# Kernel optimization log

Measured on AMD Instinct MI355X. Metric: run time of the kernel, lower is better.

Reference implementation:

```python
import jax, jax.numpy as jnp
import numpy as np

B = 16; Hp = 24; Wp = 24; N = Hp * Wp + 2  # 578 = patches + cls + freq tokens
D = 768; H = 12; HDIM = D // H
BAND = 64; SD = 16  # sd = min(16, max(4, band_dim))
HID = 3072  # int(embed_dim * mlp_ratio)
SCALE = HDIM ** -0.5; CLIP = 10.0
FILM_SCALE = 0.5; SPEC_INIT = 0.02; GATE_INIT = 0.05


def _ln(x, w, b, eps=1e-6):
    m = jnp.mean(x, axis=-1, keepdims=True)
    v = jnp.mean((x - m) ** 2, axis=-1, keepdims=True)
    return (x - m) * jax.lax.rsqrt(v + eps) * w + b


def _rms(x, eps=1e-6):
    return x * jax.lax.rsqrt(jnp.mean(x * x, axis=-1, keepdims=True) + eps)


def setup_inputs() -> dict:
    key = jax.random.key(0)
    ks = jax.random.split(key, 16)
    rn = lambda k, s, sc=1.0: jax.random.normal(k, s, dtype=jnp.float32) * sc
    return {
        "x": rn(ks[0], (B, N, D)),
        "band_tokens": rn(ks[1], (B, 1, D)),  # unused by forward (matches torch signature)
        "freq_token_for_cond": rn(ks[2], (B, 1, D)),
        "freq_summary": rn(ks[3], (B, D)),
        "token_band_feat": rn(ks[4], (B, N, BAND)),
        "alpha": jnp.ones((1,), jnp.float32),
        "ln_gate_w": jnp.ones((D,), jnp.float32), "ln_gate_b": jnp.zeros((D,), jnp.float32),
        "film_w": rn(ks[5], (D, 2 * D), 1e-4), "film_b": jnp.zeros((2 * D,), jnp.float32),
        "ln_attn_w": jnp.ones((D,), jnp.float32), "ln_attn_b": jnp.zeros((D,), jnp.float32),
        "qkv_w": rn(ks[6], (D, 3 * D), 0.02), "qkv_b": jnp.zeros((3 * D,), jnp.float32),
        "proj_w": rn(ks[7], (D, D), 0.02), "proj_b": jnp.zeros((D,), jnp.float32),
        "spec_bias_scale": jnp.float32(SPEC_INIT),
        "gate_w": rn(ks[8], (D, H), 1e-4), "gate_b": jnp.zeros((H,), jnp.float32),
        "band_proj_w": rn(ks[9], (BAND, SD), 0.02),
        "ln_mlp_w": jnp.ones((D,), jnp.float32), "ln_mlp_b": jnp.zeros((D,), jnp.float32),
        "fc1_w": rn(ks[10], (D, HID), 0.02), "fc1_b": jnp.zeros((HID,), jnp.float32),
        "fc2_w": rn(ks[11], (HID, D), 0.02), "fc2_b": jnp.zeros((D,), jnp.float32),
        "dw_w": rn(ks[12], (HID, 1, 3, 3), 0.1), "dw_b": jnp.zeros((HID,), jnp.float32),
    }


def _forward(x, band_tokens, freq_token_for_cond, freq_summary, token_band_feat, alpha,
             ln_gate_w, ln_gate_b, film_w, film_b, ln_attn_w, ln_attn_b,
             qkv_w, qkv_b, proj_w, proj_b, spec_bias_scale, gate_w, gate_b, band_proj_w,
             ln_mlp_w, ln_mlp_b, fc1_w, fc1_b, fc2_w, fc2_b, dw_w, dw_b):
    a = alpha.reshape(())
    # --- FiLM gate on patch tokens (replaces patch, no residual) ---
    cls_freq = x[:, :2]
    patch = x[:, 2:]
    p = _ln(patch, ln_gate_w, ln_gate_b)
    gb = freq_summary @ film_w + film_b            # [B, 2D]
    gamma, beta = jnp.split(gb, 2, axis=-1)
    gamma = jnp.tanh(gamma) * FILM_SCALE
    beta = jnp.tanh(beta) * FILM_SCALE
    patch = p * (1.0 + a * gamma[:, None, :]) + a * beta[:, None, :]
    x = jnp.concatenate([cls_freq, patch], axis=1)
    # --- spectral-similarity attention ---
    xn = _ln(x, ln_attn_w, ln_attn_b)
    qkv = (xn @ qkv_w + qkv_b).reshape(B, N, 3, H, HDIM)
    q = _rms(qkv[:, :, 0].transpose(0, 2, 1, 3))   # [B,H,N,hd]
    k = _rms(qkv[:, :, 1].transpose(0, 2, 1, 3))
    v = qkv[:, :, 2].transpose(0, 2, 1, 3)
    logits = jnp.einsum('bhnd,bhmd->bhnm', q * SCALE, k)
    s = _rms(token_band_feat @ band_proj_w)        # [B,N,SD]
    ssim = jnp.einsum('bns,bms->bnm', s, s)        # [B,N,N]
    logits = jnp.clip(logits + a * spec_bias_scale * ssim[:, None], -CLIP, CLIP)
    attn = jax.nn.softmax(logits, axis=-1)
    out = jnp.einsum('bhnm,bhmd->bhnd', attn, v)
    g = jnp.tanh(freq_token_for_cond[:, 0] @ gate_w + gate_b) * GATE_INIT  # [B,H]
    out = out * (1.0 + a * g[:, :, None, None])
    out = out.transpose(0, 2, 1, 3).reshape(B, N, D)
    x = x + (out @ proj_w + proj_b)
    # --- conv MLP on patch tokens only ---
    cls_freq = x[:, :2]
    patch = x[:, 2:]
    h = jax.nn.gelu(_ln(patch, ln_mlp_w, ln_mlp_b) @ fc1_w + fc1_b, approximate=False)
    h = h.transpose(0, 2, 1).reshape(B, HID, Hp, Wp)
    h = jax.lax.conv_general_dilated(h, dw_w, (1, 1), 'SAME', feature_group_count=HID,
                                     dimension_numbers=('NCHW', 'OIHW', 'NCHW'))
    h = jax.nn.silu(h + dw_b[None, :, None, None])
    h = h.reshape(B, HID, Hp * Wp).transpose(0, 2, 1)
    patch = patch + (h @ fc2_w + fc2_b)
    return jnp.concatenate([cls_freq, patch], axis=1)


def reference(x, band_tokens, freq_token_for_cond, freq_summary, token_band_feat, alpha,
              ln_gate_w, ln_gate_b, film_w, film_b, ln_attn_w, ln_attn_b,
              qkv_w, qkv_b, proj_w, proj_b, spec_bias_scale, gate_w, gate_b, band_proj_w,
              ln_mlp_w, ln_mlp_b, fc1_w, fc1_b, fc2_w, fc2_b, dw_w, dw_b):
    return _forward(x, band_tokens, freq_token_for_cond, freq_summary, token_band_feat, alpha,
                    ln_gate_w, ln_gate_b, film_w, film_b, ln_attn_w, ln_attn_b,
                    qkv_w, qkv_b, proj_w, proj_b, spec_bias_scale, gate_w, gate_b, band_proj_w,
                    ln_mlp_w, ln_mlp_b, fc1_w, fc1_b, fc2_w, fc2_b, dw_w, dw_b)
```

## Files before the change

kernel.cpp:

```cpp
#include <hip/hip_runtime.h>
#include <hip/hip_bf16.h>

#define BATCH 16
#define NTOK 578
#define NTOKP 592
#define NP 576
#define PGRID 24
#define DIM 768
#define NH 12
#define HDIM 64
#define BAND 64
#define SDIM 16
#define HID 3072
#define SCALE 0.125f
#define CLIPV 10.0f
#define KHS 104
#define VTS 72
#define PLS 72
#define FKS 16

typedef __attribute__((ext_vector_type(8))) short bf16x8;
typedef __attribute__((ext_vector_type(4))) float f32x4;

__device__ __forceinline__ float b2f(short u) {
  union { float f; unsigned int i; } x;
  x.i = ((unsigned int)(unsigned short)u) << 16;
  return x.f;
}
__device__ __forceinline__ short f2b(float x) {
  __hip_bfloat16 h = __float2bfloat16(x);
  return *reinterpret_cast<short*>(&h);
}

__device__ __forceinline__ void gload16(const short* g, short* l) {
  __builtin_amdgcn_global_load_lds(
      (const __attribute__((address_space(1))) unsigned int*)g,
      (__attribute__((address_space(3))) unsigned int*)l, 16, 0, 0);
}

__device__ __forceinline__ int swz_wgid(int orig, int nwg) {
  int xcd = orig & 7, i = orig >> 3;
  int q = nwg >> 3, r = nwg & 7;
  return (xcd < r) ? xcd * (q + 1) + i : r * (q + 1) + (xcd - r) * q + i;
}

__device__ __forceinline__ void block_reduce2(float& a, float& b) {
  __shared__ float sm[8];
  #pragma unroll
  for (int o = 32; o > 0; o >>= 1) { a += __shfl_down(a, o); b += __shfl_down(b, o); }
  int lane = threadIdx.x & 63, w = threadIdx.x >> 6;
  __syncthreads();
  if (lane == 0) { sm[w] = a; sm[4 + w] = b; }
  __syncthreads();
  a = sm[0] + sm[1] + sm[2] + sm[3];
  b = sm[4] + sm[5] + sm[6] + sm[7];
}

#define TKS 266
__device__ __forceinline__ void tw2(
    const float* __restrict__ W, short* __restrict__ Wt, int K, int N,
    int kblk, int nblk, short* t) {
  int tid = threadIdx.x;
  int k0 = kblk * 256, n0 = nblk * 64;
  int r0 = tid >> 4, c0 = (tid & 15) * 4;
  #pragma unroll
  for (int it = 0; it < 16; it++) {
    int r = it * 16 + r0;
    float4 v = *(const float4*)(W + (size_t)(k0 + r) * N + n0 + c0);
    t[(c0 + 0) * TKS + r] = f2b(v.x);
    t[(c0 + 1) * TKS + r] = f2b(v.y);
    t[(c0 + 2) * TKS + r] = f2b(v.z);
    t[(c0 + 3) * TKS + r] = f2b(v.w);
  }
  __syncthreads();
  int n1 = tid >> 5, k1 = (tid & 31) * 8;
  #pragma unroll
  for (int it = 0; it < 8; it++) {
    int n = it * 8 + n1;
    *(bf16x8*)(Wt + (size_t)(n0 + n) * K + k0 + k1) = *(bf16x8*)(t + n * TKS + k1);
  }
}

__global__ __launch_bounds__(256) void prep_weights(
    const float* __restrict__ qkv_w, const float* __restrict__ proj_w,
    const float* __restrict__ fc1_w, const float* __restrict__ fc2_w,
    const float* __restrict__ dww,
    short* __restrict__ qkvT, short* __restrict__ projT,
    short* __restrict__ fc1T, short* __restrict__ fc2T, float* __restrict__ dwt) {
  __shared__ short t[64 * TKS];
  int id = blockIdx.x;
  if (id < 108) {
    tw2(qkv_w, qkvT, 768, 2304, id % 3, id / 3, t);
  } else if (id < 144) {
    int u = id - 108; tw2(proj_w, projT, 768, 768, u % 3, u / 3, t);
  } else if (id < 288) {
    int u = id - 144; tw2(fc1_w, fc1T, 768, 3072, u % 3, u / 3, t);
  } else if (id < 432) {
    int u = id - 288; tw2(fc2_w, fc2T, 3072, 768, u % 12, u / 12, t);
  } else {
    int i = (id - 432) * 256 + threadIdx.x;
    if (i < 9 * HID) { int tt = i / HID, c = i - tt * HID; dwt[i] = dww[c * 9 + tt]; }
  }
}

__global__ __launch_bounds__(256) void film_part(
    const float* __restrict__ fsum, const float* __restrict__ film_w,
    float* __restrict__ part) {
  __shared__ float fs[BATCH][48];
  int bid = blockIdx.x;
  int cg = bid % 12, ks = bid / 12;
  int tid = threadIdx.x;
  int k0 = ks * 48;
  for (int i = tid; i < BATCH * 48; i += 256) {
    int b = i / 48, kk = i - b * 48;
    fs[b][kk] = fsum[b * DIM + k0 + kk];
  }
  __syncthreads();
  int col4 = cg * 128 + (tid & 31) * 4;
  int bq = tid >> 5;
  float a0[4] = {0.f, 0.f, 0.f, 0.f}, a1[4] = {0.f, 0.f, 0.f, 0.f};
  #pragma unroll 4
  for (int kk = 0; kk < 48; kk++) {
    float4 w = *(const float4*)(film_w + (size_t)(k0 + kk) * 2 * DIM + col4);
    float f0 = fs[bq][kk], f1 = fs[bq + 8][kk];
    a0[0] += f0 * w.x; a0[1] += f0 * w.y; a0[2] += f0 * w.z; a0[3] += f0 * w.w;
    a1[0] += f1 * w.x; a1[1] += f1 * w.y; a1[2] += f1 * w.z; a1[3] += f1 * w.w;
  }
  *(float4*)(part + ((size_t)ks * BATCH + bq) * 1536 + col4) =
      (float4){a0[0], a0[1], a0[2], a0[3]};
  *(float4*)(part + ((size_t)ks * BATCH + bq + 8) * 1536 + col4) =
      (float4){a1[0], a1[1], a1[2], a1[3]};
}

__global__ __launch_bounds__(256) void film_fin(
    const float* __restrict__ part, const float* __restrict__ film_b,
    const float* __restrict__ ftc, const float* __restrict__ gate_w,
    const float* __restrict__ gate_b,
    float* __restrict__ gamma, float* __restrict__ beta, float* __restrict__ g) {
  int bid = blockIdx.x;
  if (bid < 96) {
    int idx = bid * 256 + threadIdx.x;
    int b = idx / 1536, col = idx - b * 1536;
    float acc = film_b[col];
    #pragma unroll
    for (int ks = 0; ks < FKS; ks++)
      acc += part[((size_t)ks * BATCH + b) * 1536 + col];
    float t = tanhf(acc) * 0.5f;
    if (col < DIM) gamma[b * DIM + col] = t;
    else beta[b * DIM + (col - DIM)] = t;
  } else {
    int widx = (bid - 96) * 4 + (threadIdx.x >> 6);
    int lane = threadIdx.x & 63;
    if (widx < BATCH * NH) {
      int b = widx / NH, h = widx - b * NH;
      float acc = 0.f;
      for (int kk = lane; kk < DIM; kk += 64) acc += ftc[b * DIM + kk] * gate_w[kk * NH + h];
      #pragma unroll
      for (int o = 32; o > 0; o >>= 1) acc += __shfl_down(acc, o);
      if (lane == 0) g[widx] = tanhf(acc + gate_b[h]) * 0.05f;
    }
  }
}

__global__ __launch_bounds__(256) void band_s_kernel(
    const float* __restrict__ tbf, const float* __restrict__ bw, float* __restrict__ s) {
  int row = blockIdx.x * 4 + (threadIdx.x >> 6);
  int lane = threadIdx.x & 63;
  if (row >= BATCH * NTOK) return;
  const float* t = tbf + (size_t)row * BAND;
  float val = 0.f;
  if (lane < SDIM) {
    for (int i = 0; i < BAND; i++) val += t[i] * bw[i * SDIM + lane];
  }
  float ss = val * val;
  #pragma unroll
  for (int o = 8; o > 0; o >>= 1) ss += __shfl_xor(ss, o, 16);
  if (lane < SDIM) s[(size_t)row * SDIM + lane] = val * rsqrtf(ss * (1.f / 16.f) + 1e-6f);
}

__global__ __launch_bounds__(256) void transpose_v(
    const short* __restrict__ v, short* __restrict__ vT) {
  __shared__ short t[64][72];
  int bh = blockIdx.y;
  int n0 = blockIdx.x * 64;
  int tid = threadIdx.x;
  const short* vb = v + (size_t)bh * NTOK * HDIM;
  short* ob = vT + (size_t)bh * HDIM * NTOKP;
  {
    int r = tid >> 2, c0 = (tid & 3) * 16;
    int n = n0 + r;
    bf16x8 a0 = {0,0,0,0,0,0,0,0}, a1 = {0,0,0,0,0,0,0,0};
    if (n < NTOK) {
      a0 = *(const bf16x8*)(vb + (size_t)n * HDIM + c0);
      a1 = *(const bf16x8*)(vb + (size_t)n * HDIM + c0 + 8);
    }
    *(bf16x8*)(&t[r][c0]) = a0;
    *(bf16x8*)(&t[r][c0 + 8]) = a1;
  }
  __syncthreads();
  {
    int d = tid & 63, nc = tid >> 6;
    int nbase = n0 + nc * 16;
    short tmp[16];
    #pragma unroll
    for (int e = 0; e < 16; e++) tmp[e] = t[nc * 16 + e][d];
    if (nbase + 16 <= NTOK) {
      *(bf16x8*)(ob + (size_t)d * NTOKP + nbase) = *(bf16x8*)tmp;
      *(bf16x8*)(ob + (size_t)d * NTOKP + nbase + 8) = *(bf16x8*)(tmp + 8);
    } else {
      for (int e = 0; e < 16; e++)
        if (nbase + e < NTOK) ob[(size_t)d * NTOKP + nbase + e] = tmp[e];
    }
  }
}

__global__ __launch_bounds__(256) void ln_film_kernel(
    const float* __restrict__ x, const float* __restrict__ gamma, const float* __restrict__ beta,
    const float* __restrict__ gw, const float* __restrict__ gb,
    const float* __restrict__ aw, const float* __restrict__ ab,
    const float* __restrict__ alpha, float* __restrict__ xw, __hip_bfloat16* __restrict__ xn) {
  int row = blockIdx.x;
  int b = row / NTOK, n = row % NTOK;
  int tid = threadIdx.x;
  const float* xr = x + (size_t)row * DIM;
  float vals[3];
  #pragma unroll
  for (int j = 0; j < 3; j++) vals[j] = xr[tid + j * 256];
  if (n >= 2) {
    float s = vals[0] + vals[1] + vals[2];
    float ss = vals[0]*vals[0] + vals[1]*vals[1] + vals[2]*vals[2];
    block_reduce2(s, ss);
    float mean = s * (1.f / 768.f);
    float inv = rsqrtf(ss * (1.f / 768.f) - mean * mean + 1e-6f);
    float a = alpha[0];
    #pragma unroll
    for (int j = 0; j < 3; j++) {
      int d = tid + j * 256;
      float p = (vals[j] - mean) * inv * gw[d] + gb[d];
      vals[j] = p * (1.f + a * gamma[(size_t)b * DIM + d]) + a * beta[(size_t)b * DIM + d];
    }
  }
  float* xwr = xw + (size_t)row * DIM;
  #pragma unroll
  for (int j = 0; j < 3; j++) xwr[tid + j * 256] = vals[j];
  float s = vals[0] + vals[1] + vals[2];
  float ss = vals[0]*vals[0] + vals[1]*vals[1] + vals[2]*vals[2];
  block_reduce2(s, ss);
  float mean = s * (1.f / 768.f);
  float inv = rsqrtf(ss * (1.f / 768.f) - mean * mean + 1e-6f);
  __hip_bfloat16* xnr = xn + (size_t)row * DIM;
  #pragma unroll
  for (int j = 0; j < 3; j++) {
    int d = tid + j * 256;
    xnr[d] = __float2bfloat16((vals[j] - mean) * inv * aw[d] + ab[d]);
  }
}

__device__ __forceinline__ void stage_tile256(
    const short* __restrict__ A, const short* __restrict__ Wt, int K,
    int m0, int n0, int kt, short* Al, short* Bl, int wid, int lrow, int lcolsw) {
  #pragma unroll
  for (int it = 0; it < 4; it++) {
    int r0 = wid * 8 + it * 64;
    gload16(A + (size_t)(m0 + r0 + lrow) * K + kt + lcolsw, Al + r0 * 64);
  }
  #pragma unroll
  for (int it = 0; it < 2; it++) {
    int r0 = wid * 8 + it * 64;
    gload16(Wt + (size_t)(n0 + r0 + lrow) * K + kt + lcolsw, Bl + r0 * 64);
  }
}

__device__ __forceinline__ void compute_tile256(
    const short* Al, const short* Bl, f32x4 acc[4][4],
    int wr, int wc, int ln15, int kb) {
  int rx = ln15 & 7;
  #pragma unroll
  for (int kk = 0; kk < 2; kk++) {
    int csw = ((kk * 4 + kb) ^ rx) * 8;
    bf16x8 af[4], bfr[4];
    #pragma unroll
    for (int i = 0; i < 4; i++)
      af[i] = *(const bf16x8*)(Al + (wr * 64 + i * 16 + ln15) * 64 + csw);
    #pragma unroll
    for (int j = 0; j < 4; j++)
      bfr[j] = *(const bf16x8*)(Bl + (wc * 64 + j * 16 + ln15) * 64 + csw);
    #pragma unroll
    for (int i = 0; i < 4; i++)
      #pragma unroll
      for (int j = 0; j < 4; j++)
        acc[i][j] = __builtin_amdgcn_mfma_f32_16x16x32_bf16(af[i], bfr[j], acc[i][j], 0, 0, 0);
  }
}

__device__ __forceinline__ void mfma_core_256(
    const short* __restrict__ A, const short* __restrict__ Wt,
    int K, int m0, int n0, f32x4 acc[4][4], short* Al, short* Bl) {
  int tid = threadIdx.x, lane = tid & 63, wid = tid >> 6;
  int wr = wid >> 1, wc = wid & 1;
  int ln15 = lane & 15, kb = lane >> 4;
  int lrow = lane >> 3;
  int lcolsw = (((lane & 7) ^ lrow) & 7) * 8;
  #pragma unroll
  for (int i = 0; i < 4; i++)
    #pragma unroll
    for (int j = 0; j < 4; j++) acc[i][j] = (f32x4){0.f, 0.f, 0.f, 0.f};
  for (int kt = 0; kt < K; kt += 64) {
    stage_tile256(A, Wt, K, m0, n0, kt, Al, Bl, wid, lrow, lcolsw);
    __syncthreads();
    compute_tile256(Al, Bl, acc, wr, wc, ln15, kb);
    __syncthreads();
  }
}

__device__ __forceinline__ void stage_tile64(
    const short* __restrict__ A, const short* __restrict__ Wt, int K,
    int m0, int n0, int kt, short* Al, short* Bl, int wid, int lrow, int lcolsw) {
  #pragma unroll
  for (int it = 0; it < 2; it++) {
    int r0 = wid * 8 + it * 32;
    gload16(A + (size_t)(m0 + r0 + lrow) * K + kt + lcolsw, Al + r0 * 64);
  }
  #pragma unroll
  for (int it = 0; it < 4; it++) {
    int r0 = wid * 8 + it * 32;
    gload16(Wt + (size_t)(n0 + r0 + lrow) * K + kt + lcolsw, Bl + r0 * 64);
  }
}

__device__ __forceinline__ void compute_tile64(
    const short* Al, const short* Bl, f32x4 acc[4][2],
    int wid, int ln15, int kb) {
  int rx = ln15 & 7;
  #pragma unroll
  for (int kk = 0; kk < 2; kk++) {
    int csw = ((kk * 4 + kb) ^ rx) * 8;
    bf16x8 af[4], bfr[2];
    #pragma unroll
    for (int i = 0; i < 4; i++)
      af[i] = *(const bf16x8*)(Al + (i * 16 + ln15) * 64 + csw);
    #pragma unroll
    for (int j = 0; j < 2; j++)
      bfr[j] = *(const bf16x8*)(Bl + (wid * 32 + j * 16 + ln15) * 64 + csw);
    #pragma unroll
    for (int i = 0; i < 4; i++)
      #pragma unroll
      for (int j = 0; j < 2; j++)
        acc[i][j] = __builtin_amdgcn_mfma_f32_16x16x32_bf16(af[i], bfr[j], acc[i][j], 0, 0, 0);
  }
}

__device__ __forceinline__ void mfma_core_64(
    const short* __restrict__ A, const short* __restrict__ Wt,
    int K, int m0, int n0, f32x4 acc[4][2],
    short* Al0, short* Bl0, short* Al1, short* Bl1) {
  int tid = threadIdx.x, lane = tid & 63, wid = tid >> 6;
  int ln15 = lane & 15, kb = lane >> 4;
  int lrow = lane >> 3;
  int lcolsw = (((lane & 7) ^ lrow) & 7) * 8;
  #pragma unroll
  for (int i = 0; i < 4; i++)
    #pragma unroll
    for (int j = 0; j < 2; j++) acc[i][j] = (f32x4){0.f, 0.f, 0.f, 0.f};
  stage_tile64(A, Wt, K, m0, n0, 0, Al0, Bl0, wid, lrow, lcolsw);
  stage_tile64(A, Wt, K, m0, n0, 64, Al1, Bl1, wid, lrow, lcolsw);
  asm volatile("s_waitcnt vmcnt(6)" ::: "memory");
  __builtin_amdgcn_s_barrier();
  const int NKT = K >> 6;
  for (int t = 0; t < NKT; t++) {
    const short* Ac = (t & 1) ? Al1 : Al0;
    const short* Bc = (t & 1) ? Bl1 : Bl0;
    compute_tile64(Ac, Bc, acc, wid, ln15, kb);
    __builtin_amdgcn_s_barrier();
    if (t + 2 < NKT) {
      short* As = (t & 1) ? Al1 : Al0;
      short* Bs = (t & 1) ? Bl1 : Bl0;
      stage_tile64(A, Wt, K, m0, n0, (t + 2) << 6, As, Bs, wid, lrow, lcolsw);
      asm volatile("s_waitcnt vmcnt(6)" ::: "memory");
    } else if (t + 1 < NKT) {
      asm volatile("s_waitcnt vmcnt(0)" ::: "memory");
    }
    __builtin_amdgcn_s_barrier();
  }
}

__global__ __launch_bounds__(512) void gemm_qkv(
    const short* __restrict__ A, const short* __restrict__ Wt, const float* __restrict__ bias,
    __hip_bfloat16* __restrict__ q, __hip_bfloat16* __restrict__ k, __hip_bfloat16* __restrict__ v) {
  __shared__ short Al[256 * 64], Bl[128 * 64];
  f32x4 acc[4][4];
  int wgid = swz_wgid(blockIdx.x, 37 * 18);
  int m0 = (wgid % 37) * 256, n0 = (wgid / 37) * 128;
  mfma_core_256(A, Wt, DIM, m0, n0, acc, Al, Bl);
  int tid = threadIdx.x, lane = tid & 63, wid = tid >> 6, wr = wid >> 1, wc = wid & 1;
  int ln15 = lane & 15, lq = lane >> 4;
  int colbase = n0 + wc * 64;
  int which = colbase / DIM;
  int rem = colbase - which * DIM;
  int h = rem >> 6;
  __hip_bfloat16* dst = (which == 0) ? q : ((which == 1) ? k : v);
  float fin_scale = (which == 0) ? SCALE : 1.0f;
  float bv[4];
  #pragma unroll
  for (int j = 0; j < 4; j++) bv[j] = bias[colbase + j * 16 + ln15];
  #pragma unroll
  for (int i = 0; i < 4; i++) {
    #pragma unroll
    for (int r = 0; r < 4; r++) {
      int m = m0 + wr * 64 + i * 16 + lq * 4 + r;
      float v4[4];
      #pragma unroll
      for (int j = 0; j < 4; j++) v4[j] = acc[i][j][r] + bv[j];
      float inv = fin_scale;
      if (which < 2) {
        float ss = v4[0]*v4[0] + v4[1]*v4[1] + v4[2]*v4[2] + v4[3]*v4[3];
        ss += __shfl_xor(ss, 1); ss += __shfl_xor(ss, 2);
        ss += __shfl_xor(ss, 4); ss += __shfl_xor(ss, 8);
        inv = rsqrtf(ss * (1.f / 64.f) + 1e-6f) * fin_scale;
      }
      if (m < BATCH * NTOK) {
        int b = m / NTOK, n = m - b * NTOK;
        __hip_bfloat16* orow = dst + (((size_t)b * NH + h) * NTOK + n) * HDIM;
        #pragma unroll
        for (int j = 0; j < 4; j++)
          orow[j * 16 + ln15] = __float2bfloat16(v4[j] * inv);
      }
    }
  }
}

__global__ __launch_bounds__(512) void attn_mfma(
    const short* __restrict__ q, const short* __restrict__ k,
    const short* __restrict__ vT, const float* __restrict__ s,
    const float* __restrict__ g, const float* __restrict__ alpha,
    const float* __restrict__ sbs, short* __restrict__ ao) {
  __shared__ short Kh[64 * KHS];
  __shared__ short Vt[2][64 * VTS];
  __shared__ short Pl[8][16 * PLS];
  int xcd = blockIdx.x & 7, idx = blockIdx.x >> 3;
  int bh = xcd * 24 + idx / 5;
  int n0 = (idx % 5) * 128;
  int b = bh / NH, h = bh - b * NH;
  int tid = threadIdx.x, lane = tid & 63, w = tid >> 6;
  int l15 = lane & 15, lg = lane >> 4;
  float a = alpha[0], c = a * sbs[0];
  const short* qb = q + (size_t)bh * NTOK * HDIM;
  const short* kb = k + (size_t)bh * NTOK * HDIM;
  const short* vtb = vT + (size_t)bh * HDIM * NTOKP;
  const float* sb = s + (size_t)b * NTOK * SDIM;
  const bf16x8 Z8 = {0, 0, 0, 0, 0, 0, 0, 0};

  int qrow = n0 + w * 16 + l15;
  int qsrc = (qrow < NTOK) ? qrow : 0;
  bf16x8 qf0 = *(const bf16x8*)(qb + (size_t)qsrc * HDIM + lg * 8);
  bf16x8 qf1 = *(const bf16x8*)(qb + (size_t)qsrc * HDIM + 32 + lg * 8);
  bf16x8 qf2 = Z8;
  if (lg < 2) {
    const float* sp = sb + (size_t)qsrc * SDIM + lg * 8;
    #pragma unroll
    for (int j = 0; j < 8; j++) qf2[j] = f2b(c * sp[j]);
  }

  f32x4 accO[4];
  #pragma unroll
  for (int dd = 0; dd < 4; dd++) accO[dd] = (f32x4){0.f, 0.f, 0.f, 0.f};
  float rsum[4] = {0.f, 0.f, 0.f, 0.f};

  int srow = (tid & 255) >> 2, sseg = tid & 3;
  if (tid < 256 && sseg == 3) {
    short* dst = Kh + srow * KHS + 80;
    *(bf16x8*)dst = Z8;
    *(bf16x8*)(dst + 8) = Z8;
  }

  auto stageK = [&](int mt) {
    int key = mt + srow;
    bool kok = key < NTOK;
    if (sseg < 2) {
      bf16x8 v0 = Z8, v1 = Z8, v2 = Z8, v3 = Z8;
      if (kok) {
        const short* src = kb + (size_t)key * HDIM + sseg * 32;
        v0 = *(const bf16x8*)(src);
        v1 = *(const bf16x8*)(src + 8);
        v2 = *(const bf16x8*)(src + 16);
        v3 = *(const bf16x8*)(src + 24);
      }
      short* dst = Kh + srow * KHS + sseg * 32;
      *(bf16x8*)dst = v0;
      *(bf16x8*)(dst + 8) = v1;
      *(bf16x8*)(dst + 16) = v2;
      *(bf16x8*)(dst + 24) = v3;
    } else if (sseg == 2) {
      bf16x8 v0 = Z8, v1 = Z8;
      if (kok) {
        const float* sp = sb + (size_t)key * SDIM;
        #pragma unroll
        for (int j = 0; j < 8; j++) { v0[j] = f2b(sp[j]); v1[j] = f2b(sp[j + 8]); }
      }
      short* dst = Kh + srow * KHS + 64;
      *(bf16x8*)dst = v0;
      *(bf16x8*)(dst + 8) = v1;
    }
  };
  auto stageV = [&](int mt, short* VtB) {
    int kk0 = sseg * 16;
    short* dst = VtB + srow * VTS + kk0;
    const short* src = vtb + (size_t)srow * NTOKP + mt + kk0;
    if (mt + kk0 + 16 <= NTOK) {
      *(bf16x8*)dst = *(const bf16x8*)src;
      *(bf16x8*)(dst + 8) = *(const bf16x8*)(src + 8);
    } else {
      for (int e = 0; e < 16; e++)
        dst[e] = (mt + kk0 + e < NTOK) ? src[e] : (short)0;
    }
  };

  if (tid < 256) stageK(0); else stageV(0, Vt[0]);
  __syncthreads();
  const int NT = 10;
  for (int ti = 0; ti < NT; ti++) {
    int mt = ti * 64, cur = ti & 1;
    const short* VtC = Vt[cur];
    f32x4 sa[4];
    __builtin_amdgcn_s_setprio(1);
    #pragma unroll
    for (int jj = 0; jj < 4; jj++) {
      sa[jj] = (f32x4){0.f, 0.f, 0.f, 0.f};
      const short* kp = Kh + (jj * 16 + l15) * KHS + lg * 8;
      sa[jj] = __builtin_amdgcn_mfma_f32_16x16x32_bf16(qf0, *(const bf16x8*)kp, sa[jj], 0, 0, 0);
      sa[jj] = __builtin_amdgcn_mfma_f32_16x16x32_bf16(qf1, *(const bf16x8*)(kp + 32), sa[jj], 0, 0, 0);
      sa[jj] = __builtin_amdgcn_mfma_f32_16x16x32_bf16(qf2, *(const bf16x8*)(kp + 64), sa[jj], 0, 0, 0);
    }
    __builtin_amdgcn_s_setprio(0);
    __syncthreads();
    if (ti + 1 < NT) {
      if (tid < 256) stageK(mt + 64);
      else stageV(mt + 64, Vt[cur ^ 1]);
    }
    short* pw = Pl[w];
    float ps[4][4];
    #pragma unroll
    for (int jj = 0; jj < 4; jj++) {
      bool ok = (mt + jj * 16 + l15) < NTOK;
      #pragma unroll
      for (int r = 0; r < 4; r++) {
        float x = sa[jj][r];
        x = fminf(fmaxf(x, -CLIPV), CLIPV);
        float e = ok ? __expf(x) : 0.f;
        ps[jj][r] = e;
        pw[(lg * 4 + r) * PLS + jj * 16 + l15] = f2b(e);
      }
    }
    #pragma unroll
    for (int r = 0; r < 4; r++) {
      float t = ps[0][r] + ps[1][r] + ps[2][r] + ps[3][r];
      t += __shfl_xor(t, 1); t += __shfl_xor(t, 2);
      t += __shfl_xor(t, 4); t += __shfl_xor(t, 8);
      rsum[r] += t;
    }
    __builtin_amdgcn_s_setprio(1);
    #pragma unroll
    for (int kc = 0; kc < 2; kc++) {
      bf16x8 pa = *(const bf16x8*)(pw + l15 * PLS + kc * 32 + lg * 8);
      #pragma unroll
      for (int dd = 0; dd < 4; dd++) {
        bf16x8 vf = *(const bf16x8*)(VtC + (dd * 16 + l15) * VTS + kc * 32 + lg * 8);
        accO[dd] = __builtin_amdgcn_mfma_f32_16x16x32_bf16(pa, vf, accO[dd], 0, 0, 0);
      }
    }
    __builtin_amdgcn_s_setprio(0);
    __syncthreads();
  }
  float gm = 1.f + a * g[bh];
  #pragma unroll
  for (int r = 0; r < 4; r++) {
    int n = n0 + w * 16 + lg * 4 + r;
    if (n >= NTOK) continue;
    float inv = gm / rsum[r];
    short* orow = ao + ((size_t)b * NTOK + n) * DIM + h * HDIM;
    #pragma unroll
    for (int dd = 0; dd < 4; dd++)
      orow[dd * 16 + l15] = f2b(accO[dd][r] * inv);
  }
}

__global__ __launch_bounds__(256) void gemm_proj(
    const short* __restrict__ A, const short* __restrict__ Wt, const float* __restrict__ bias,
    float* __restrict__ xw, float* __restrict__ out) {
  __shared__ short Al0[64 * 64], Bl0[128 * 64], Al1[64 * 64], Bl1[128 * 64];
  f32x4 acc[4][2];
  int wgid = swz_wgid(blockIdx.x, 145 * 6);
  int m0 = (wgid % 145) * 64, n0 = (wgid / 145) * 128;
  mfma_core_64(A, Wt, DIM, m0, n0, acc, Al0, Bl0, Al1, Bl1);
  int tid = threadIdx.x, lane = tid & 63, wid = tid >> 6;
  int ln15 = lane & 15, lq = lane >> 4;
  #pragma unroll
  for (int i = 0; i < 4; i++) {
    #pragma unroll
    for (int j = 0; j < 2; j++) {
      int col = n0 + wid * 32 + j * 16 + ln15;
      float bv = bias[col];
      #pragma unroll
      for (int r = 0; r < 4; r++) {
        int m = m0 + i * 16 + lq * 4 + r;
        if (m >= BATCH * NTOK) continue;
        int n = m % NTOK;
        float val = acc[i][j][r] + bv + xw[(size_t)m * DIM + col];
        xw[(size_t)m * DIM + col] = val;
        if (n < 2) out[(size_t)m * DIM + col] = val;
      }
    }
  }
}

__global__ __launch_bounds__(256) void ln_mlp_kernel(
    const float* __restrict__ x2, const float* __restrict__ w, const float* __restrict__ bb,
    __hip_bfloat16* __restrict__ xm) {
  int r = blockIdx.x;
  int b = r / NP, pi = r % NP;
  int tid = threadIdx.x;
  const float* xr = x2 + ((size_t)b * NTOK + 2 + pi) * DIM;
  float vals[3];
  #pragma unroll
  for (int j = 0; j < 3; j++) vals[j] = xr[tid + j * 256];
  float s = vals[0] + vals[1] + vals[2];
  float ss = vals[0]*vals[0] + vals[1]*vals[1] + vals[2]*vals[2];
  block_reduce2(s, ss);
  float mean = s * (1.f / 768.f);
  float inv = rsqrtf(ss * (1.f / 768.f) - mean * mean + 1e-6f);
  __hip_bfloat16* xo = xm + (size_t)r * DIM;
  #pragma unroll
  for (int j = 0; j < 3; j++) {
    int d = tid + j * 256;
    xo[d] = __float2bfloat16((vals[j] - mean) * inv * w[d] + bb[d]);
  }
}

__global__ __launch_bounds__(512) void gemm_fc1(
    const short* __restrict__ A, const short* __restrict__ Wt, const float* __restrict__ bias,
    __hip_bfloat16* __restrict__ h1) {
  __shared__ short Al[256 * 64], Bl[128 * 64];
  f32x4 acc[4][4];
  int wgid = swz_wgid(blockIdx.x, 18 * 24);
  int m0 = (wgid % 18) * 256, n0 = (wgid / 18) * 128;
  mfma_core_256(A, Wt, DIM, m0, n0, acc, Al, Bl);
  int tid = threadIdx.x, lane = tid & 63, wid = tid >> 6, wr = wid >> 1, wc = wid & 1;
  int ln15 = lane & 15, lq = lane >> 4;
  #pragma unroll
  for (int i = 0; i < 4; i++) {
    #pragma unroll
    for (int j = 0; j < 4; j++) {
      int col = n0 + wc * 64 + j * 16 + ln15;
      float bv = bias[col];
      #pragma unroll
      for (int r = 0; r < 4; r++) {
        int m = m0 + wr * 64 + i * 16 + lq * 4 + r;
        float val = acc[i][j][r] + bv;
        float ge = 0.5f * val * (1.f + erff(val * 0.70710678118f));
        h1[(size_t)m * HID + col] = __float2bfloat16(ge);
      }
    }
  }
}

__global__ __launch_bounds__(256) void dwconv_kernel(
    const __hip_bfloat16* __restrict__ h1, const float* __restrict__ dwt,
    const float* __restrict__ dwb, __hip_bfloat16* __restrict__ h2) {
  int gx = blockIdx.x;
  int b = gx / 144, g = gx - b * 144;
  int y = g / 6, x0 = (g - y * 6) * 4;
  int tid = threadIdx.x;
  int c0 = blockIdx.y * 512 + (tid & 63) * 8;
  int x = x0 + (tid >> 6);
  const short* in = (const short*)h1 + (size_t)b * NP * HID + c0;
  bf16x8 iv[3][3];
  #pragma unroll
  for (int ky = 0; ky < 3; ky++) {
    int yy = y + ky - 1;
    #pragma unroll
    for (int kx = 0; kx < 3; kx++) {
      int xx = x + kx - 1;
      bool ok = (yy >= 0 && yy < PGRID && xx >= 0 && xx < PGRID);
      iv[ky][kx] = ok ? *(const bf16x8*)(in + (size_t)(yy * PGRID + xx) * HID)
                      : (bf16x8){0, 0, 0, 0, 0, 0, 0, 0};
    }
  }
  float acc[8];
  {
    float4 b0 = *(const float4*)(dwb + c0);
    float4 b1 = *(const float4*)(dwb + c0 + 4);
    acc[0] = b0.x; acc[1] = b0.y; acc[2] = b0.z; acc[3] = b0.w;
    acc[4] = b1.x; acc[5] = b1.y; acc[6] = b1.z; acc[7] = b1.w;
  }
  #pragma unroll
  for (int t = 0; t < 9; t++) {
    float4 w0 = *(const float4*)(dwt + t * HID + c0);
    float4 w1 = *(const float4*)(dwt + t * HID + c0 + 4);
    bf16x8 xv = iv[t / 3][t % 3];
    acc[0] += b2f(xv[0]) * w0.x; acc[1] += b2f(xv[1]) * w0.y;
    acc[2] += b2f(xv[2]) * w0.z; acc[3] += b2f(xv[3]) * w0.w;
    acc[4] += b2f(xv[4]) * w1.x; acc[5] += b2f(xv[5]) * w1.y;
    acc[6] += b2f(xv[6]) * w1.z; acc[7] += b2f(xv[7]) * w1.w;
  }
  short ov[8];
  #pragma unroll
  for (int e = 0; e < 8; e++) {
    float v = acc[e];
    ov[e] = f2b(v / (1.f + __expf(-v)));
  }
  *(bf16x8*)((short*)h2 + ((size_t)b * NP + y * PGRID + x) * HID + c0) = *(bf16x8*)ov;
}

__global__ __launch_bounds__(256) void gemm_fc2(
    const short* __restrict__ A, const short* __restrict__ Wt, const float* __restrict__ bias,
    const float* __restrict__ xw, float* __restrict__ out, int b0) {
  __shared__ short Al0[64 * 64], Bl0[128 * 64], Al1[64 * 64], Bl1[128 * 64];
  f32x4 acc[4][2];
  int wgid = swz_wgid(blockIdx.x, 72 * 6);
  int m0 = (wgid % 72) * 64, n0 = (wgid / 72) * 128;
  mfma_core_64(A, Wt, HID, m0, n0, acc, Al0, Bl0, Al1, Bl1);
  int tid = threadIdx.x, lane = tid & 63, wid = tid >> 6;
  int ln15 = lane & 15, lq = lane >> 4;
  #pragma unroll
  for (int i = 0; i < 4; i++) {
    #pragma unroll
    for (int j = 0; j < 2; j++) {
      int col = n0 + wid * 32 + j * 16 + ln15;
      float bv = bias[col];
      #pragma unroll
      for (int r = 0; r < 4; r++) {
        int m = m0 + i * 16 + lq * 4 + r;
        int bl = m / NP, pi = m - bl * NP;
        size_t orow = ((size_t)(b0 + bl) * NTOK + 2 + pi) * DIM;
        out[orow + col] = acc[i][j][r] + bv + xw[orow + col];
      }
    }
  }
}

extern "C" void kernel_launch(void* const* d_in, const int* in_sizes, int n_in,
                              void* d_out, int out_size, void* d_ws, size_t ws_size,
                              hipStream_t stream) {
  const float* x      = (const float*)d_in[0];
  const float* ftc    = (const float*)d_in[2];
  const float* fsum   = (const float*)d_in[3];
  const float* tbf    = (const float*)d_in[4];
  const float* alpha  = (const float*)d_in[5];
  const float* lgw    = (const float*)d_in[6];
  const float* lgb    = (const float*)d_in[7];
  const float* film_w = (const float*)d_in[8];
  const float* film_b = (const float*)d_in[9];
  const float* law    = (const float*)d_in[10];
  const float* lab    = (const float*)d_in[11];
  const float* qkv_w  = (const float*)d_in[12];
  const float* qkv_b  = (const float*)d_in[13];
  const float* proj_w = (const float*)d_in[14];
  const float* proj_b = (const float*)d_in[15];
  const float* sbs    = (const float*)d_in[16];
  const float* gate_w = (const float*)d_in[17];
  const float* gate_b = (const float*)d_in[18];
  const float* band_w = (const float*)d_in[19];
  const float* lmw    = (const float*)d_in[20];
  const float* lmb    = (const float*)d_in[21];
  const float* fc1_w  = (const float*)d_in[22];
  const float* fc1_b  = (const float*)d_in[23];
  const float* fc2_w  = (const float*)d_in[24];
  const float* fc2_b  = (const float*)d_in[25];
  const float* dw_w   = (const float*)d_in[26];
  const float* dw_b   = (const float*)d_in[27];
  float* out = (float*)d_out;

  float* ws = (float*)d_ws;
  const size_t SZ = (size_t)BATCH * NTOK * DIM;

  float* p_xw = ws;
  short* p_xn = (short*)(ws + SZ);
  short* p_q  = (short*)(ws + SZ + SZ / 2);
  short* p_k  = (short*)(ws + 2 * SZ);
  short* p_v  = (short*)(ws + 2 * SZ + SZ / 2);
  float* p_s  = ws + 3 * SZ;
  float* p_gamma = p_s + (size_t)BATCH * NTOK * SDIM;
  float* p_beta  = p_gamma + BATCH * DIM;
  float* p_g     = p_beta + BATCH * DIM;
  float* p_dwt   = p_g + 256;
  float* p_part  = p_dwt + 9 * HID;
  float* wtb = p_part + (size_t)FKS * BATCH * 1536;
  short* qkvT = (short*)wtb;
  short* projT = qkvT + (size_t)768 * 2304;
  short* fc1T  = projT + (size_t)768 * 768;
  short* fc2T  = fc1T + (size_t)768 * 3072;
  short* h2c   = fc2T + (size_t)3072 * 768;

  const size_t total_floats =
      3 * SZ + (size_t)BATCH * NTOK * SDIM + 2 * (size_t)BATCH * DIM + 256 + 9 * HID +
      (size_t)FKS * BATCH * 1536 +
      ((size_t)768 * 2304 + 768 * 768 + 768 * 3072 + 3072 * 768) / 2 +
      ((size_t)8 * NP * HID) / 2;
  if (ws_size < total_floats * sizeof(float)) return;

  short* p_ao = p_xn;
  short* p_xm = p_q;
  short* h1c  = p_k;
  short* p_vT = h2c;

  dim3 blk(256);

  prep_weights<<<dim3(432 + 108), blk, 0, stream>>>(
      qkv_w, proj_w, fc1_w, fc2_w, dw_w, qkvT, projT, fc1T, fc2T, p_dwt);

  film_part<<<dim3(12 * FKS), blk, 0, stream>>>(fsum, film_w, p_part);

  film_fin<<<dim3(96 + 48), blk, 0, stream>>>(
      p_part, film_b, ftc, gate_w, gate_b, p_gamma, p_beta, p_g);

  band_s_kernel<<<dim3((BATCH * NTOK + 3) / 4), blk, 0, stream>>>(tbf, band_w, p_s);

  ln_film_kernel<<<dim3(BATCH * NTOK), blk, 0, stream>>>(
      x, p_gamma, p_beta, lgw, lgb, law, lab, alpha, p_xw, (__hip_bfloat16*)p_xn);

  gemm_qkv<<<dim3(37 * 18), dim3(512), 0, stream>>>(
      p_xn, qkvT, qkv_b, (__hip_bfloat16*)p_q, (__hip_bfloat16*)p_k, (__hip_bfloat16*)p_v);

  transpose_v<<<dim3(10, BATCH * NH), blk, 0, stream>>>(p_v, p_vT);

  attn_mfma<<<dim3(960), dim3(512), 0, stream>>>(
      p_q, p_k, p_vT, p_s, p_g, alpha, sbs, p_ao);

  gemm_proj<<<dim3(145 * 6), blk, 0, stream>>>(p_ao, projT, proj_b, p_xw, out);

  ln_mlp_kernel<<<dim3(BATCH * NP), blk, 0, stream>>>(p_xw, lmw, lmb, (__hip_bfloat16*)p_xm);

  for (int cc = 0; cc < 2; cc++) {
    const short* Ach = p_xm + (size_t)cc * 4608 * DIM;
    gemm_fc1<<<dim3(18 * 24), dim3(512), 0, stream>>>(Ach, fc1T, fc1_b, (__hip_bfloat16*)h1c);
    dwconv_kernel<<<dim3(8 * 144, 6), blk, 0, stream>>>(
        (const __hip_bfloat16*)h1c, p_dwt, dw_b, (__hip_bfloat16*)h2c);
    gemm_fc2<<<dim3(72 * 6), blk, 0, stream>>>(h2c, fc2T, fc2_b, p_xw, out, cc * 8);
  }
}
```

Before: 443.5 us.

## Double-buffer K tiles and prefetch next K/V tile into registers in attention

```diff
diff --git a/kernel.cpp b/kernel.cpp
--- a/kernel.cpp
+++ b/kernel.cpp
@@ -434,7 +434,7 @@
     const short* __restrict__ vT, const float* __restrict__ s,
     const float* __restrict__ g, const float* __restrict__ alpha,
     const float* __restrict__ sbs, short* __restrict__ ao) {
-  __shared__ short Kh[64 * KHS];
+  __shared__ short Kh[2][64 * KHS];
   __shared__ short Vt[2][64 * VTS];
   __shared__ short Pl[8][16 * PLS];
   int xcd = blockIdx.x & 7, idx = blockIdx.x >> 3;
@@ -468,13 +468,16 @@
 
   int srow = (tid & 255) >> 2, sseg = tid & 3;
   if (tid < 256 && sseg == 3) {
-    short* dst = Kh + srow * KHS + 80;
-    *(bf16x8*)dst = Z8;
-    *(bf16x8*)(dst + 8) = Z8;
-  }
-
-  auto stageK = [&](int mt) {
-    int key = mt + srow;
+    #pragma unroll
+    for (int bb = 0; bb < 2; bb++) {
+      short* dst = Kh[bb] + srow * KHS + 80;
+      *(bf16x8*)dst = Z8;
+      *(bf16x8*)(dst + 8) = Z8;
+    }
+  }
+
+  if (tid < 256) {
+    int key = srow;
     bool kok = key < NTOK;
     if (sseg < 2) {
       bf16x8 v0 = Z8, v1 = Z8, v2 = Z8, v3 = Z8;
@@ -485,7 +488,7 @@
         v2 = *(const bf16x8*)(src + 16);
         v3 = *(const bf16x8*)(src + 24);
       }
-      short* dst = Kh + srow * KHS + sseg * 32;
+      short* dst = Kh[0] + srow * KHS + sseg * 32;
       *(bf16x8*)dst = v0;
       *(bf16x8*)(dst + 8) = v1;
       *(bf16x8*)(dst + 16) = v2;
@@ -497,45 +500,91 @@
         #pragma unroll
         for (int j = 0; j < 8; j++) { v0[j] = f2b(sp[j]); v1[j] = f2b(sp[j + 8]); }
       }
-      short* dst = Kh + srow * KHS + 64;
+      short* dst = Kh[0] + srow * KHS + 64;
       *(bf16x8*)dst = v0;
       *(bf16x8*)(dst + 8) = v1;
     }
-  };
-  auto stageV = [&](int mt, short* VtB) {
+  } else {
     int kk0 = sseg * 16;
-    short* dst = VtB + srow * VTS + kk0;
-    const short* src = vtb + (size_t)srow * NTOKP + mt + kk0;
-    if (mt + kk0 + 16 <= NTOK) {
-      *(bf16x8*)dst = *(const bf16x8*)src;
-      *(bf16x8*)(dst + 8) = *(const bf16x8*)(src + 8);
-    } else {
-      for (int e = 0; e < 16; e++)
-        dst[e] = (mt + kk0 + e < NTOK) ? src[e] : (short)0;
-    }
-  };
-
-  if (tid < 256) stageK(0); else stageV(0, Vt[0]);
+    const short* src = vtb + (size_t)srow * NTOKP + kk0;
+    short* dst = Vt[0] + srow * VTS + kk0;
+    *(bf16x8*)dst = *(const bf16x8*)src;
+    *(bf16x8*)(dst + 8) = *(const bf16x8*)(src + 8);
+  }
   __syncthreads();
+
   const int NT = 10;
   for (int ti = 0; ti < NT; ti++) {
     int mt = ti * 64, cur = ti & 1;
+    const short* KhC = Kh[cur];
     const short* VtC = Vt[cur];
+    bool nxt = (ti + 1 < NT);
+    int mtn = mt + 64;
+    bf16x8 kr0 = Z8, kr1 = Z8, kr2 = Z8, kr3 = Z8;
+    float4 sf0 = {0,0,0,0}, sf1 = {0,0,0,0}, sf2 = {0,0,0,0}, sf3 = {0,0,0,0};
+    if (nxt) {
+      if (tid < 256) {
+        int key = mtn + srow;
+        bool kok = key < NTOK;
+        if (sseg < 2) {
+          if (kok) {
+            const short* src = kb + (size_t)key * HDIM + sseg * 32;
+            kr0 = *(const bf16x8*)(src);
+            kr1 = *(const bf16x8*)(src + 8);
+            kr2 = *(const bf16x8*)(src + 16);
+            kr3 = *(const bf16x8*)(src + 24);
+          }
+        } else if (sseg == 2) {
+          if (kok) {
+            const float* sp = sb + (size_t)key * SDIM;
+            sf0 = *(const float4*)(sp);
+            sf1 = *(const float4*)(sp + 4);
+            sf2 = *(const float4*)(sp + 8);
+            sf3 = *(const float4*)(sp + 12);
+          }
+        }
+      } else {
+        int kk0 = sseg * 16;
+        const short* src = vtb + (size_t)srow * NTOKP + mtn + kk0;
+        kr0 = *(const bf16x8*)src;
+        kr1 = *(const bf16x8*)(src + 8);
+      }
+    }
     f32x4 sa[4];
     __builtin_amdgcn_s_setprio(1);
     #pragma unroll
     for (int jj = 0; jj < 4; jj++) {
       sa[jj] = (f32x4){0.f, 0.f, 0.f, 0.f};
-      const short* kp = Kh + (jj * 16 + l15) * KHS + lg * 8;
+      const short* kp = KhC + (jj * 16 + l15) * KHS + lg * 8;
       sa[jj] = __builtin_amdgcn_mfma_f32_16x16x32_bf16(qf0, *(const bf16x8*)kp, sa[jj], 0, 0, 0);
       sa[jj] = __builtin_amdgcn_mfma_f32_16x16x32_bf16(qf1, *(const bf16x8*)(kp + 32), sa[jj], 0, 0, 0);
       sa[jj] = __builtin_amdgcn_mfma_f32_16x16x32_bf16(qf2, *(const bf16x8*)(kp + 64), sa[jj], 0, 0, 0);
     }
     __builtin_amdgcn_s_setprio(0);
-    __syncthreads();
-    if (ti + 1 < NT) {
-      if (tid < 256) stageK(mt + 64);
-      else stageV(mt + 64, Vt[cur ^ 1]);
+    if (nxt) {
+      if (tid < 256) {
+        if (sseg < 2) {
+          short* dst = Kh[cur ^ 1] + srow * KHS + sseg * 32;
+          *(bf16x8*)dst = kr0;
+          *(bf16x8*)(dst + 8) = kr1;
+          *(bf16x8*)(dst + 16) = kr2;
+          *(bf16x8*)(dst + 24) = kr3;
+        } else if (sseg == 2) {
+          bf16x8 v0, v1;
+          v0[0] = f2b(sf0.x); v0[1] = f2b(sf0.y); v0[2] = f2b(sf0.z); v0[3] = f2b(sf0.w);
+          v0[4] = f2b(sf1.x); v0[5] = f2b(sf1.y); v0[6] = f2b(sf1.z); v0[7] = f2b(sf1.w);
+          v1[0] = f2b(sf2.x); v1[1] = f2b(sf2.y); v1[2] = f2b(sf2.z); v1[3] = f2b(sf2.w);
+          v1[4] = f2b(sf3.x); v1[5] = f2b(sf3.y); v1[6] = f2b(sf3.z); v1[7] = f2b(sf3.w);
+          short* dst = Kh[cur ^ 1] + srow * KHS + 64;
+          *(bf16x8*)dst = v0;
+          *(bf16x8*)(dst + 8) = v1;
+        }
+      } else {
+        int kk0 = sseg * 16;
+        short* dst = Vt[cur ^ 1] + srow * VTS + kk0;
+        *(bf16x8*)dst = kr0;
+        *(bf16x8*)(dst + 8) = kr1;
+      }
     }
     short* pw = Pl[w];
     float ps[4][4];
```

Measured after the change: 438.5 us. No clear change (-1.1%).
